# Optimization experiments

Measured on AMD Instinct MI355X. Metric: run time of the kernel, lower is better.

The kernel has to match this reference:

```python
import jax, jax.numpy as jnp
import numpy as np
from jax import lax

TEMPERATURE = 30.0
PAD = 1  # padding init-kwarg; stride=1, dilation=1


def setup_inputs() -> dict:
    key = jax.random.key(0)
    ks = jax.random.split(key, 8)
    B, D, HID, NF, K, CIN, COUT, HW = 32, 512, 256, 8, 3, 64, 64, 64
    return {
        "filter_condition_input": jax.random.normal(ks[0], (B, D), jnp.float32),
        "model_input": jax.random.normal(ks[1], (B, CIN, HW, HW), jnp.float32),
        "fc1_w": jax.random.normal(ks[2], (HID, D), jnp.float32) * (2.0 / D) ** 0.5,
        "fc1_b": jnp.zeros((HID,), jnp.float32),
        "fc2_w": jax.random.normal(ks[3], (NF, HID), jnp.float32) * (2.0 / HID) ** 0.5,
        "fc2_b": jnp.zeros((NF,), jnp.float32),
        "weight": jax.random.normal(ks[4], (NF, COUT, CIN, K, K), jnp.float32) * 0.05,
        "bias_p": jax.random.normal(ks[5], (NF, COUT), jnp.float32) * 0.05,
    }


def reference(filter_condition_input, model_input, fc1_w, fc1_b, fc2_w, fc2_b, weight, bias_p):
    # Routing MLP -> softmax attention over the num_filters kernel bank
    h = jax.nn.relu(filter_condition_input @ fc1_w.T + fc1_b)
    logits = h @ fc2_w.T + fc2_b
    attn = jax.nn.softmax(logits / TEMPERATURE, axis=1)  # [B, NF]

    # Per-sample aggregated conv kernels and biases
    agg_w = jnp.einsum("bf,foikl->boikl", attn, weight)  # [B, O, Cin, K, K]
    agg_b = attn @ bias_p                                  # [B, O]

    # groups = batch_size grouped conv == independent per-sample conv (vmapped)
    def conv1(x_i, w_i):  # x_i: [Cin,H,W], w_i: [O,Cin,K,K]
        return lax.conv_general_dilated(
            x_i[None], w_i, window_strides=(1, 1),
            padding=((PAD, PAD), (PAD, PAD)),
            dimension_numbers=("NCHW", "OIHW", "NCHW"))[0]

    out = jax.vmap(conv1)(model_input, agg_w) + agg_b[:, :, None, None]  # [B,O,H,W]
    return out, attn
```

## Files before the change

### kernel.cpp

```cpp
#include <hip/hip_runtime.h>
#include <hip/hip_bf16.h>

typedef __hip_bfloat16 bf16;
typedef unsigned short u16;
typedef unsigned int   u32;

#define B_    32
#define D_    512
#define HID_  256
#define NF_   8
#define CIN_  64
#define COUT_ 64
#define HW_   64
#define CONV_OUT_ELEMS (B_ * COUT_ * HW_ * HW_)
#define WBANK_ (NF_ * 36864)

typedef __attribute__((ext_vector_type(8))) short  short8;
typedef __attribute__((ext_vector_type(4))) float  floatx4;

__device__ inline float b2f(bf16 v) { return __bfloat162float(v); }
__device__ inline bf16  f2b(float f) { return __float2bfloat16(f); }
__device__ inline u16 f2bu(float f) { union { bf16 h; u16 u; } c; c.h = __float2bfloat16(f); return c.u; }
__device__ inline float bu2f(u16 u) { union { u32 i; float f; } c; c.i = ((u32)u) << 16; return c.f; }

__device__ inline int detect_bf16(const void* p, int elems) {
    const u32* w = (const u32*)p;
    int nw = elems >> 1;
    if (nw < 1) return 1;
    int n = nw < 32 ? nw : 32;
    int step = nw / n;
    int ok = 1;
#pragma unroll 8
    for (int k = 0; k < n; ++k) {
        u32 v = w[k * step];
        u32 lo = v & 0xFFFFu;
        u32 ex = (lo >> 7) & 0xFFu;
        if (!(lo == 0u || (ex >= 64u && ex <= 191u))) ok = 0;
    }
    return ok;
}

__device__ inline float ldf(const void* p, int i, int isbf) {
    return isbf ? __bfloat162float(((const bf16*)p)[i]) : ((const float*)p)[i];
}

__global__ __launch_bounds__(256) void routing_kernel(
    const void* __restrict__ x, const void* __restrict__ xin,
    const void* __restrict__ fc1_w, const void* __restrict__ fc1_b,
    const void* __restrict__ fc2_w, const void* __restrict__ fc2_b,
    const void* __restrict__ bias_p,
    float* __restrict__ ws_attn, float* __restrict__ ws_aggb,
    void* __restrict__ d_out)
{
    __shared__ float xs[D_];
    __shared__ float hs[HID_];
    __shared__ float at[NF_];
    __shared__ int   fl[7];
    const int b = blockIdx.x;
    const int t = threadIdx.x;

    if (t == 0) {
        fl[0] = detect_bf16(x,      B_ * D_);
        fl[1] = detect_bf16(fc1_w,  HID_ * D_);
        fl[2] = detect_bf16(fc1_b,  HID_);
        fl[3] = detect_bf16(fc2_w,  NF_ * HID_);
        fl[4] = detect_bf16(fc2_b,  NF_);
        fl[5] = detect_bf16(bias_p, NF_ * COUT_);
        fl[6] = detect_bf16(xin,    B_ * CIN_ * HW_ * HW_);
    }
    __syncthreads();

    for (int i = t; i < D_; i += 256) xs[i] = ldf(x, b * D_ + i, fl[0]);
    __syncthreads();

    {
        float s = 0.f;
        if (fl[1]) {
            const uint4* row = (const uint4*)((const bf16*)fc1_w + t * D_);
#pragma unroll 4
            for (int i = 0; i < D_ / 8; ++i) {
                uint4 u = row[i];
                const float* xp = xs + i * 8;
                s += bu2f((u16)(u.x & 0xFFFF)) * xp[0] + bu2f((u16)(u.x >> 16)) * xp[1]
                   + bu2f((u16)(u.y & 0xFFFF)) * xp[2] + bu2f((u16)(u.y >> 16)) * xp[3]
                   + bu2f((u16)(u.z & 0xFFFF)) * xp[4] + bu2f((u16)(u.z >> 16)) * xp[5]
                   + bu2f((u16)(u.w & 0xFFFF)) * xp[6] + bu2f((u16)(u.w >> 16)) * xp[7];
            }
        } else {
            const float4* row = (const float4*)((const float*)fc1_w + t * D_);
#pragma unroll 4
            for (int i = 0; i < D_ / 4; ++i) {
                float4 u = row[i];
                const float* xp = xs + i * 4;
                s += u.x * xp[0] + u.y * xp[1] + u.z * xp[2] + u.w * xp[3];
            }
        }
        s += ldf(fc1_b, t, fl[2]);
        hs[t] = s > 0.f ? s : 0.f;
    }
    __syncthreads();

    if (t < NF_) {
        float s = ldf(fc2_b, t, fl[4]);
        const int base = t * HID_;
        for (int j = 0; j < HID_; ++j) s += hs[j] * ldf(fc2_w, base + j, fl[3]);
        at[t] = s * (1.0f / 30.0f);
    }
    __syncthreads();
    if (t == 0) {
        float m = at[0];
#pragma unroll
        for (int f = 1; f < NF_; ++f) m = fmaxf(m, at[f]);
        float e[NF_], ssum = 0.f;
#pragma unroll
        for (int f = 0; f < NF_; ++f) { e[f] = __expf(at[f] - m); ssum += e[f]; }
        float inv = 1.0f / ssum;
#pragma unroll
        for (int f = 0; f < NF_; ++f) at[f] = e[f] * inv;
    }
    __syncthreads();
    if (t < NF_) {
        ws_attn[b * NF_ + t] = at[t];
        if (fl[6]) ((bf16*)d_out)[CONV_OUT_ELEMS + b * NF_ + t] = f2b(at[t]);
        else      ((float*)d_out)[CONV_OUT_ELEMS + b * NF_ + t] = at[t];
    }
    if (t < COUT_) {
        float s = 0.f;
#pragma unroll
        for (int f = 0; f < NF_; ++f) s += at[f] * ldf(bias_p, f * COUT_ + t, fl[5]);
        ws_aggb[b * COUT_ + t] = s;
    }
}

__global__ __launch_bounds__(256) void agg_kernel(
    const void* __restrict__ weight,
    const float* __restrict__ ws_attn,
    u16* __restrict__ aggw)
{
    __shared__ float lds[2304];
    __shared__ float s_at[NF_];
    __shared__ int   s_wbf;
    const int t  = threadIdx.x;
    const int b  = blockIdx.x >> 4;
    const int o0 = (blockIdx.x & 15) * 4;

    if (t == 0) s_wbf = detect_bf16(weight, WBANK_);
    if (t < NF_) s_at[t] = ws_attn[b * NF_ + t];
    __syncthreads();
    const int wbf = s_wbf;

#pragma unroll
    for (int j = 0; j < 9; ++j) {
        const int flat = t + 256 * j;
        const int o_l = flat / 576, rr = flat - o_l * 576;
        const int gbase = (o0 + o_l) * 576 + rr;
        float s = 0.f;
        if (wbf) {
#pragma unroll
            for (int f = 0; f < NF_; ++f) s += s_at[f] * b2f(((const bf16*)weight)[f * 36864 + gbase]);
        } else {
#pragma unroll
            for (int f = 0; f < NF_; ++f) s += s_at[f] * ((const float*)weight)[f * 36864 + gbase];
        }
        lds[flat] = s;
    }
    __syncthreads();
#pragma unroll
    for (int j = 0; j < 9; ++j) {
        const int e = t + 256 * j;
        const int tap = e >> 8, o_l = (e >> 6) & 3, ci = e & 63;
        aggw[b * 36864 + tap * 4096 + (o0 + o_l) * 64 + ci] = f2bu(lds[o_l * 576 + ci * 9 + tap]);
    }
}

__global__ __launch_bounds__(256, 2) void conv_mfma(
    const void* __restrict__ xin,
    const u16*  __restrict__ aggw,
    const float* __restrict__ aggb,
    void* __restrict__ out)
{
    __shared__ __align__(16) u16 smem[31104];
    __shared__ float bias_s[COUT_];
    __shared__ int s_ok;
    u16* in_s = smem;
    u16* w_s  = smem + 12672;

    const int t    = threadIdx.x;
    const int bz   = blockIdx.x;
    const int b    = bz >> 4;
    const int y0   = (bz & 15) * 4;
    const int wv   = t >> 6;
    const int lane = t & 63, l15 = lane & 15, q = lane >> 4;

    if (t == 0) s_ok = 1;
    __syncthreads();
    if (t < 32) {
        u32 w = ((const u32*)xin)[t * 131072];
        u32 lo = w & 0xFFFFu, ex = (lo >> 7) & 0xFFu;
        if (!(lo == 0u || (ex >= 64u && ex <= 191u))) atomicAnd(&s_ok, 0);
    }
    if (t < COUT_) bias_s[t] = aggb[b * COUT_ + t];
    __syncthreads();
    const int inbf = s_ok;

    floatx4 acc[4][4];
#pragma unroll
    for (int mt = 0; mt < 4; ++mt)
#pragma unroll
        for (int nt = 0; nt < 4; ++nt) acc[mt][nt] = (floatx4)0.f;

    for (int ph = 0; ph < 2; ++ph) {
        const int ci0 = ph * 32;
        __syncthreads();
#pragma unroll
        for (int j = 0; j < 9; ++j) {
            const int item = t + 256 * j;
            const int o = item & 63, cib = (item >> 6) & 3, tap = item >> 8;
            uint4 v = *(const uint4*)(aggw + b * 36864 + tap * 4096 + o * 64 + ci0 + cib * 8);
            *(uint4*)&w_s[((tap * 4 + cib) * 64 + o) * 8] = v;
        }
#pragma unroll
        for (int j = 0; j < 3; ++j) {
            const int item = t + 256 * j;
            const int cp = item & 15, z = item >> 4;
            const int r = z % 6, ch = z / 6;
            const int gy = y0 - 1 + r, gx0 = ch * 8;
            const int ci = ci0 + cp * 2;
            union { uint4 v; u16 s[8]; } a0, a1;
            if (gy >= 0 && gy < HW_) {
                const int gi = ((b * CIN_ + ci) * HW_ + gy) * HW_ + gx0;
                if (inbf) {
                    a0.v = *(const uint4*)((const bf16*)xin + gi);
                    a1.v = *(const uint4*)((const bf16*)xin + gi + HW_ * HW_);
                } else {
                    const float* p0 = (const float*)xin + gi;
                    const float* p1 = p0 + HW_ * HW_;
                    float4 f00 = *(const float4*)p0, f01 = *(const float4*)(p0 + 4);
                    float4 f10 = *(const float4*)p1, f11 = *(const float4*)(p1 + 4);
                    a0.s[0]=f2bu(f00.x); a0.s[1]=f2bu(f00.y); a0.s[2]=f2bu(f00.z); a0.s[3]=f2bu(f00.w);
                    a0.s[4]=f2bu(f01.x); a0.s[5]=f2bu(f01.y); a0.s[6]=f2bu(f01.z); a0.s[7]=f2bu(f01.w);
                    a1.s[0]=f2bu(f10.x); a1.s[1]=f2bu(f10.y); a1.s[2]=f2bu(f10.z); a1.s[3]=f2bu(f10.w);
                    a1.s[4]=f2bu(f11.x); a1.s[5]=f2bu(f11.y); a1.s[6]=f2bu(f11.z); a1.s[7]=f2bu(f11.w);
                }
            } else {
                a0.v = make_uint4(0,0,0,0); a1.v = make_uint4(0,0,0,0);
            }
            const int cib = cp >> 2, p = cp & 3;
            u32* dst = (u32*)in_s;
#pragma unroll
            for (int k = 0; k < 8; ++k) {
                const int col = 1 + gx0 + k;
                dst[((r * 4 + cib) * 66 + col) * 4 + p] = (u32)a0.s[k] | ((u32)a1.s[k] << 16);
            }
        }
        if (t < 192) {
            const int cp = t & 15, z = t >> 4;
            const int r = z % 6, col = (z / 6) ? 65 : 0;
            ((u32*)in_s)[((r * 4 + (cp >> 2)) * 66 + col) * 4 + (cp & 3)] = 0u;
        }
        __syncthreads();
#pragma unroll
        for (int tap = 0; tap < 9; ++tap) {
            const int kh = tap / 3, kw = tap % 3;
            short8 af[4], bfr[4];
#pragma unroll
            for (int mt = 0; mt < 4; ++mt)
                af[mt] = *(const short8*)&w_s[((tap * 4 + q) * 64 + mt * 16 + l15) * 8];
#pragma unroll
            for (int nt = 0; nt < 4; ++nt)
                bfr[nt] = *(const short8*)&in_s[(((wv + kh) * 4 + q) * 66 + nt * 16 + l15 + kw) * 8];
#pragma unroll
            for (int mt = 0; mt < 4; ++mt)
#pragma unroll
                for (int nt = 0; nt < 4; ++nt)
                    acc[mt][nt] = __builtin_amdgcn_mfma_f32_16x16x32_bf16(af[mt], bfr[nt], acc[mt][nt], 0, 0, 0);
        }
    }

    __syncthreads();
    u16* out_s = smem;
#pragma unroll
    for (int mt = 0; mt < 4; ++mt) {
        floatx4 bb = *(const floatx4*)&bias_s[mt * 16 + q * 4];
#pragma unroll
        for (int nt = 0; nt < 4; ++nt) {
#pragma unroll
            for (int rg = 0; rg < 4; ++rg) {
                const float v = acc[mt][nt][rg] + bb[rg];
                out_s[(wv * 64 + (mt * 16 + q * 4 + rg)) * 68 + nt * 16 + l15] = f2bu(v);
            }
        }
    }
    __syncthreads();
    const int outbf = inbf;
#pragma unroll
    for (int j = 0; j < 16; ++j) {
        const int c = t + 256 * j;
        const int x0 = (c & 15) * 4, o = (c >> 4) & 63, w2 = c >> 10;
        const u16* src = &out_s[(w2 * 64 + o) * 68 + x0];
        const u16 h0 = src[0], h1 = src[1], h2 = src[2], h3 = src[3];
        const int gidx = ((b * COUT_ + o) * HW_ + (y0 + w2)) * HW_ + x0;
        if (outbf) {
            uint2 pk; pk.x = (u32)h0 | ((u32)h1 << 16); pk.y = (u32)h2 | ((u32)h3 << 16);
            *(uint2*)((u16*)out + gidx) = pk;
        } else {
            float4 f; f.x = bu2f(h0); f.y = bu2f(h1); f.z = bu2f(h2); f.w = bu2f(h3);
            *(float4*)((float*)out + gidx) = f;
        }
    }
}

extern "C" void kernel_launch(void* const* d_in, const int* in_sizes, int n_in,
                              void* d_out, int out_size, void* d_ws, size_t ws_size,
                              hipStream_t stream) {
    const void* x      = d_in[0];
    const void* xin    = d_in[1];
    const void* fc1_w  = d_in[2];
    const void* fc1_b  = d_in[3];
    const void* fc2_w  = d_in[4];
    const void* fc2_b  = d_in[5];
    const void* weight = d_in[6];
    const void* bias_p = d_in[7];

    float* ws      = (float*)d_ws;
    float* ws_attn = ws;
    float* ws_aggb = ws + 256;
    u16*   ws_aggw = (u16*)(ws + 2304);

    routing_kernel<<<dim3(B_), dim3(256), 0, stream>>>(
        x, xin, fc1_w, fc1_b, fc2_w, fc2_b, bias_p, ws_attn, ws_aggb, d_out);

    agg_kernel<<<dim3(B_ * 16), dim3(256), 0, stream>>>(weight, ws_attn, ws_aggw);

    conv_mfma<<<dim3(B_ * 16), dim3(256), 0, stream>>>(xin, ws_aggw, ws_aggb, d_out);
}
```

Measured before the change: 159.3 us.

## Parallelize dtype detection and routing MLP across warps with shuffle reductions

New measurement: 164.5 us. 1.03x slower.

```diff
diff --git a/kernel.cpp b/kernel.cpp
--- a/kernel.cpp
+++ b/kernel.cpp
@@ -23,25 +23,14 @@
 __device__ inline u16 f2bu(float f) { union { bf16 h; u16 u; } c; c.h = __float2bfloat16(f); return c.u; }
 __device__ inline float bu2f(u16 u) { union { u32 i; float f; } c; c.i = ((u32)u) << 16; return c.f; }
 
-__device__ inline int detect_bf16(const void* p, int elems) {
-    const u32* w = (const u32*)p;
-    int nw = elems >> 1;
-    if (nw < 1) return 1;
-    int n = nw < 32 ? nw : 32;
-    int step = nw / n;
-    int ok = 1;
-#pragma unroll 8
-    for (int k = 0; k < n; ++k) {
-        u32 v = w[k * step];
-        u32 lo = v & 0xFFFFu;
-        u32 ex = (lo >> 7) & 0xFFu;
-        if (!(lo == 0u || (ex >= 64u && ex <= 191u))) ok = 0;
-    }
-    return ok;
-}
-
 __device__ inline float ldf(const void* p, int i, int isbf) {
     return isbf ? __bfloat162float(((const bf16*)p)[i]) : ((const float*)p)[i];
+}
+
+__device__ inline int word_bf16_sane(u32 v) {
+    u32 lo = v & 0xFFFFu;
+    u32 ex = (lo >> 7) & 0xFFu;
+    return (lo == 0u || (ex >= 64u && ex <= 191u)) ? 1 : 0;
 }
 
 __global__ __launch_bounds__(256) void routing_kernel(
@@ -55,58 +44,72 @@
     __shared__ float xs[D_];
     __shared__ float hs[HID_];
     __shared__ float at[NF_];
-    __shared__ int   fl[7];
+    __shared__ int   fl[8];
     const int b = blockIdx.x;
     const int t = threadIdx.x;
-
-    if (t == 0) {
-        fl[0] = detect_bf16(x,      B_ * D_);
-        fl[1] = detect_bf16(fc1_w,  HID_ * D_);
-        fl[2] = detect_bf16(fc1_b,  HID_);
-        fl[3] = detect_bf16(fc2_w,  NF_ * HID_);
-        fl[4] = detect_bf16(fc2_b,  NF_);
-        fl[5] = detect_bf16(bias_p, NF_ * COUT_);
-        fl[6] = detect_bf16(xin,    B_ * CIN_ * HW_ * HW_);
-    }
-    __syncthreads();
-
-    for (int i = t; i < D_; i += 256) xs[i] = ldf(x, b * D_ + i, fl[0]);
-    __syncthreads();
-
-    {
-        float s = 0.f;
-        if (fl[1]) {
-            const uint4* row = (const uint4*)((const bf16*)fc1_w + t * D_);
-#pragma unroll 4
-            for (int i = 0; i < D_ / 8; ++i) {
-                uint4 u = row[i];
-                const float* xp = xs + i * 8;
-                s += bu2f((u16)(u.x & 0xFFFF)) * xp[0] + bu2f((u16)(u.x >> 16)) * xp[1]
-                   + bu2f((u16)(u.y & 0xFFFF)) * xp[2] + bu2f((u16)(u.y >> 16)) * xp[3]
-                   + bu2f((u16)(u.z & 0xFFFF)) * xp[4] + bu2f((u16)(u.z >> 16)) * xp[5]
-                   + bu2f((u16)(u.w & 0xFFFF)) * xp[6] + bu2f((u16)(u.w >> 16)) * xp[7];
-            }
+    const int w = t >> 6, l = t & 63;
+
+    if (t < 8) fl[t] = 1;
+    __syncthreads();
+    if (t < 224) {
+        const void* bufs[7]  = { x, fc1_w, fc1_b, fc2_w, fc2_b, bias_p, xin };
+        const int   elems[7] = { B_ * D_, HID_ * D_, HID_, NF_ * HID_, NF_,
+                                 NF_ * COUT_, B_ * CIN_ * HW_ * HW_ };
+        const int g = t >> 5, k = t & 31;
+        const int nw = elems[g] >> 1;
+        const int n = nw < 32 ? nw : 32;
+        if (k < n && nw >= 1) {
+            const int step = nw / n;
+            u32 v = ((const u32*)bufs[g])[k * step];
+            if (!word_bf16_sane(v)) atomicAnd(&fl[g], 0);
+        }
+    }
+    __syncthreads();
+    const int xbf = fl[0], w1bf = fl[1], b1bf = fl[2], w2bf = fl[3];
+    const int b2bf = fl[4], bpbf = fl[5], obf = fl[6];
+
+    for (int i = t; i < D_; i += 256) xs[i] = ldf(x, b * D_ + i, xbf);
+    __syncthreads();
+
+    const float* xp = xs + l * 8;
+#pragma unroll 2
+    for (int hi = 0; hi < 64; ++hi) {
+        const int h = w * 64 + hi;
+        float p;
+        if (w1bf) {
+            uint4 u = *(const uint4*)((const bf16*)fc1_w + h * D_ + l * 8);
+            p = bu2f((u16)(u.x & 0xFFFF)) * xp[0] + bu2f((u16)(u.x >> 16)) * xp[1]
+              + bu2f((u16)(u.y & 0xFFFF)) * xp[2] + bu2f((u16)(u.y >> 16)) * xp[3]
+              + bu2f((u16)(u.z & 0xFFFF)) * xp[4] + bu2f((u16)(u.z >> 16)) * xp[5]
+              + bu2f((u16)(u.w & 0xFFFF)) * xp[6] + bu2f((u16)(u.w >> 16)) * xp[7];
         } else {
-            const float4* row = (const float4*)((const float*)fc1_w + t * D_);
-#pragma unroll 4
-            for (int i = 0; i < D_ / 4; ++i) {
-                float4 u = row[i];
-                const float* xp = xs + i * 4;
-                s += u.x * xp[0] + u.y * xp[1] + u.z * xp[2] + u.w * xp[3];
-            }
-        }
-        s += ldf(fc1_b, t, fl[2]);
-        hs[t] = s > 0.f ? s : 0.f;
-    }
-    __syncthreads();
-
-    if (t < NF_) {
-        float s = ldf(fc2_b, t, fl[4]);
-        const int base = t * HID_;
-        for (int j = 0; j < HID_; ++j) s += hs[j] * ldf(fc2_w, base + j, fl[3]);
-        at[t] = s * (1.0f / 30.0f);
-    }
-    __syncthreads();
+            const float* r = (const float*)fc1_w + h * D_ + l * 8;
+            float4 a = *(const float4*)r, c = *(const float4*)(r + 4);
+            p = a.x * xp[0] + a.y * xp[1] + a.z * xp[2] + a.w * xp[3]
+              + c.x * xp[4] + c.y * xp[5] + c.z * xp[6] + c.w * xp[7];
+        }
+#pragma unroll
+        for (int m = 32; m; m >>= 1) p += __shfl_xor(p, m);
+        if (l == 0) {
+            p += ldf(fc1_b, h, b1bf);
+            hs[h] = p > 0.f ? p : 0.f;
+        }
+    }
+    __syncthreads();
+
+#pragma unroll
+    for (int ff = 0; ff < 2; ++ff) {
+        const int f = w * 2 + ff;
+        float p = 0.f;
+#pragma unroll
+        for (int j = 0; j < 4; ++j)
+            p += hs[j * 64 + l] * ldf(fc2_w, f * HID_ + j * 64 + l, w2bf);
+#pragma unroll
+        for (int m = 32; m; m >>= 1) p += __shfl_xor(p, m);
+        if (l == 0) at[f] = (p + ldf(fc2_b, f, b2bf)) * (1.0f / 30.0f);
+    }
+    __syncthreads();
+
     if (t == 0) {
         float m = at[0];
 #pragma unroll
@@ -121,13 +124,13 @@
     __syncthreads();
     if (t < NF_) {
         ws_attn[b * NF_ + t] = at[t];
-        if (fl[6]) ((bf16*)d_out)[CONV_OUT_ELEMS + b * NF_ + t] = f2b(at[t]);
-        else      ((float*)d_out)[CONV_OUT_ELEMS + b * NF_ + t] = at[t];
+        if (obf) ((bf16*)d_out)[CONV_OUT_ELEMS + b * NF_ + t] = f2b(at[t]);
+        else    ((float*)d_out)[CONV_OUT_ELEMS + b * NF_ + t] = at[t];
     }
     if (t < COUT_) {
         float s = 0.f;
 #pragma unroll
-        for (int f = 0; f < NF_; ++f) s += at[f] * ldf(bias_p, f * COUT_ + t, fl[5]);
+        for (int f = 0; f < NF_; ++f) s += at[f] * ldf(bias_p, f * COUT_ + t, bpbf);
         ws_aggb[b * COUT_ + t] = s;
     }
 }
@@ -144,8 +147,14 @@
     const int b  = blockIdx.x >> 4;
     const int o0 = (blockIdx.x & 15) * 4;
 
-    if (t == 0) s_wbf = detect_bf16(weight, WBANK_);
+    if (t == 0) s_wbf = 1;
     if (t < NF_) s_at[t] = ws_attn[b * NF_ + t];
+    __syncthreads();
+    if (t < 32) {
+        const int nw = WBANK_ >> 1, step = nw / 32;
+        u32 v = ((const u32*)weight)[t * step];
+        if (!word_bf16_sane(v)) atomicAnd(&s_wbf, 0);
+    }
     __syncthreads();
     const int wbf = s_wbf;
 
@@ -196,8 +205,7 @@
     __syncthreads();
     if (t < 32) {
         u32 w = ((const u32*)xin)[t * 131072];
-        u32 lo = w & 0xFFFFu, ex = (lo >> 7) & 0xFFu;
-        if (!(lo == 0u || (ex >= 64u && ex <= 191u))) atomicAnd(&s_ok, 0);
+        if (!word_bf16_sane(w)) atomicAnd(&s_ok, 0);
     }
     if (t < COUT_) bias_s[t] = aggb[b * COUT_ + t];
     __syncthreads();
```
